# Kernel tuning notes

Hardware: AMD Instinct MI355X
Metric: run time of the kernel (lower is better)

Reference implementation:

```python
import math
import jax, jax.numpy as jnp
import numpy as np

V, S, D, H, L, DS = 256, 1024, 768, 12, 4, 3
B = 4
PEN, EW, FW, RW = 1.0, 0.01, 0.01, 0.01


def setup_inputs():
    ks = jax.random.split(jax.random.key(0), 12)
    std = 0.02
    return {
        "idx": jax.random.randint(ks[0], (B, S), 0, V),
        "targets": jax.random.randint(ks[1], (B, S), 0, V),
        "token_emb": jax.random.normal(ks[2], (V, D)) * std,
        "pos_emb": jax.random.normal(ks[3], (S, D)) * std,
        "token_positions": jax.random.normal(ks[4], (V, DS)) * 0.3,
        "pos_proj_w": jax.random.normal(ks[5], (DS, D)) * std,
        "ln1_g": jnp.ones((L, D)), "ln1_b": jnp.zeros((L, D)),
        "Wqkv": jax.random.normal(ks[6], (L, D, 3 * D)) * std,
        "Wproj": jax.random.normal(ks[7], (L, D, D)) * std,
        "ln2_g": jnp.ones((L, D)), "ln2_b": jnp.zeros((L, D)),
        "Wff1": jax.random.normal(ks[8], (L, D, 4 * D)) * std,
        "bff1": jnp.zeros((L, 4 * D)),
        "Wff2": jax.random.normal(ks[9], (L, 4 * D, D)) * std,
        "bff2": jnp.zeros((L, D)),
        "lnf_g": jnp.ones((D,)), "lnf_b": jnp.zeros((D,)),
    }


def _ln(x, g, b, eps=1e-5):
    m = x.mean(-1, keepdims=True)
    v = ((x - m) ** 2).mean(-1, keepdims=True)
    return (x - m) * jax.lax.rsqrt(v + eps) * g + b


def _forward(idx, targets, p):
    Bv, T = idx.shape
    dh = D // H
    x = p["token_emb"][idx] + p["pos_emb"][jnp.arange(T)]
    seq_pos = p["token_positions"][idx]  # (B,T,3)
    diff = seq_pos[:, :, None, :] - seq_pos[:, None, :, :]
    token_dists = jnp.sqrt((diff ** 2).sum(-1) + 1e-12)  # (B,T,T)
    x = x + seq_pos @ p["pos_proj_w"]
    mask = jnp.triu(jnp.ones((T, T), dtype=bool), k=1)

    def block(carry, lp):
        x, de, fe = carry
        ln1g, ln1b, Wqkv, Wproj, ln2g, ln2b, W1, b1, W2, b2 = lp
        h = _ln(x, ln1g, ln1b)
        q, k, v = jnp.split(h @ Wqkv, 3, axis=-1)
        q = q.reshape(Bv, T, H, dh).transpose(0, 2, 1, 3)
        k = k.reshape(Bv, T, H, dh).transpose(0, 2, 1, 3)
        v = v.reshape(Bv, T, H, dh).transpose(0, 2, 1, 3)
        logits = jnp.einsum('bhid,bhjd->bhij', q, k) / math.sqrt(dh)
        logits = logits - PEN * token_dists[:, None]
        logits = jnp.where(mask, -jnp.inf, logits)
        w = jax.nn.softmax(logits, axis=-1)  # (B,H,T,T)
        de = de + (w * token_dists[:, None]).sum(-1).mean()
        fe = fe + (-(w * jnp.log(w + 1e-9)).sum(-1)).mean()
        o = jnp.einsum('bhij,bhjd->bhid', w, v).transpose(0, 2, 1, 3).reshape(Bv, T, D)
        x = x + o @ Wproj
        h2 = _ln(x, ln2g, ln2b)
        x = x + jax.nn.gelu(h2 @ W1 + b1, approximate=False) @ W2 + b2
        return (x, de, fe), None

    lps = (p["ln1_g"], p["ln1_b"], p["Wqkv"], p["Wproj"], p["ln2_g"], p["ln2_b"],
           p["Wff1"], p["bff1"], p["Wff2"], p["bff2"])
    zero = jnp.zeros((), x.dtype)
    (x, de, fe), _ = jax.lax.scan(block, (x, zero, zero), lps)
    x = _ln(x, p["lnf_g"], p["lnf_b"])
    logits = x @ p["token_emb"].T  # tied lm_head
    pv = p["token_positions"]
    dmat = jnp.sqrt(((pv[:, None] - pv[None]) ** 2).sum(-1) + 1e-12)
    off = ~jnp.eye(V, dtype=bool)
    rep = jnp.where(off, 1.0 / (dmat + 1e-4), 0.0).sum() / (V * (V - 1))
    logp = jax.nn.log_softmax(logits, -1)
    ce = -jnp.take_along_axis(logp, targets[..., None], -1).mean()
    loss = ce + EW * de + FW * fe + RW * rep
    return logits, loss, de, fe, rep


PNAMES = ("token_emb", "pos_emb", "token_positions", "pos_proj_w", "ln1_g", "ln1_b",
          "Wqkv", "Wproj", "ln2_g", "ln2_b", "Wff1", "bff1", "Wff2", "bff2", "lnf_g", "lnf_b")


def reference(idx, targets, token_emb, pos_emb, token_positions, pos_proj_w,
              ln1_g, ln1_b, Wqkv, Wproj, ln2_g, ln2_b,
              Wff1, bff1, Wff2, bff2, lnf_g, lnf_b):
    p = dict(zip(PNAMES, (token_emb, pos_emb, token_positions, pos_proj_w, ln1_g, ln1_b,
                          Wqkv, Wproj, ln2_g, ln2_b, Wff1, bff1, Wff2, bff2, lnf_g, lnf_b)))
    return _forward(idx, targets, p)
```

## Files before the change

kernel.cpp:

```cpp
#include <hip/hip_runtime.h>
#include <math.h>

#define V_   256
#define S_   1024
#define D_   768
#define H_   12
#define L_   4
#define DS_  3
#define B_   4
#define DH_  64
#define BS_  (B_*S_)
#define D3_  (3*D_)
#define D4_  (4*D_)
#define BSV_ (BS_*V_)

typedef __attribute__((ext_vector_type(8))) short short8;
typedef __attribute__((ext_vector_type(4))) float f32x4;

__device__ __forceinline__ ushort f2bf(float f) {
    unsigned u = __float_as_uint(f);
    u = (u + 0x7fffu + ((u >> 16) & 1u)) >> 16;
    return (ushort)u;
}

__device__ __forceinline__ float block_sum(float v, float* red) {
    #pragma unroll
    for (int m = 32; m > 0; m >>= 1) v += __shfl_xor(v, m, 64);
    int wid = threadIdx.x >> 6;
    __syncthreads();
    if ((threadIdx.x & 63) == 0) red[wid] = v;
    __syncthreads();
    return red[0] + red[1] + red[2] + red[3];
}

__device__ __forceinline__ float block_max(float v, float* red) {
    #pragma unroll
    for (int m = 32; m > 0; m >>= 1) v = fmaxf(v, __shfl_xor(v, m, 64));
    int wid = threadIdx.x >> 6;
    __syncthreads();
    if ((threadIdx.x & 63) == 0) red[wid] = v;
    __syncthreads();
    return fmaxf(fmaxf(red[0], red[1]), fmaxf(red[2], red[3]));
}

__global__ void zero_kernel(float* acc) {
    if (threadIdx.x < 8) acc[threadIdx.x] = 0.0f;
}

__global__ __launch_bounds__(256) void embed_kernel(
    const int* __restrict__ idx, const float* __restrict__ tok_emb,
    const float* __restrict__ pos_emb, const float* __restrict__ tok_pos,
    const float* __restrict__ pproj, float* __restrict__ x, float* __restrict__ sp)
{
    int r = blockIdx.x;
    int t = r & (S_ - 1);
    int id = idx[r];
    float s0 = tok_pos[id*3+0], s1 = tok_pos[id*3+1], s2 = tok_pos[id*3+2];
    if (threadIdx.x == 0) { sp[r*3+0] = s0; sp[r*3+1] = s1; sp[r*3+2] = s2; }
    for (int d = threadIdx.x; d < D_; d += 256) {
        x[(size_t)r*D_ + d] = tok_emb[(size_t)id*D_ + d] + pos_emb[(size_t)t*D_ + d]
                            + s0*pproj[d] + s1*pproj[D_+d] + s2*pproj[2*D_+d];
    }
}

template<int OUT>
__global__ __launch_bounds__(256) void ln_kernel(
    const float* __restrict__ in, const float* __restrict__ g,
    const float* __restrict__ b, void* __restrict__ outv)
{
    __shared__ float red[4];
    int r = blockIdx.x, tid = threadIdx.x;
    const float* p = in + (size_t)r*D_;
    float v0 = p[tid], v1 = p[tid+256], v2 = p[tid+512];
    float s = block_sum(v0+v1+v2, red);
    float mean = s * (1.0f/768.0f);
    float d0 = v0-mean, d1 = v1-mean, d2 = v2-mean;
    float var = block_sum(d0*d0+d1*d1+d2*d2, red) * (1.0f/768.0f);
    float inv = rsqrtf(var + 1e-5f);
    float o0 = d0*inv*g[tid    ] + b[tid    ];
    float o1 = d1*inv*g[tid+256] + b[tid+256];
    float o2 = d2*inv*g[tid+512] + b[tid+512];
    if (OUT == 0) {
        float* o = (float*)outv + (size_t)r*D_;
        o[tid] = o0; o[tid+256] = o1; o[tid+512] = o2;
    } else {
        ushort* o = (ushort*)outv + (size_t)r*D_;
        o[tid] = f2bf(o0); o[tid+256] = f2bf(o1); o[tid+512] = f2bf(o2);
    }
}

__global__ __launch_bounds__(256) void transpose_bf16_kernel(
    const float* __restrict__ W, ushort* __restrict__ Wt, int K, int N)
{
    __shared__ float t[32][33];
    int n0 = blockIdx.x * 32, k0 = blockIdx.y * 32;
    int tx = threadIdx.x & 31, ty = threadIdx.x >> 5;
    #pragma unroll
    for (int r = 0; r < 32; r += 8)
        t[ty+r][tx] = W[(size_t)(k0+ty+r)*N + n0 + tx];
    __syncthreads();
    #pragma unroll
    for (int r = 0; r < 32; r += 8)
        Wt[(size_t)(n0+ty+r)*K + k0 + tx] = f2bf(t[tx][ty+r]);
}

template<int EPI>
__global__ __launch_bounds__(256) void gemm_bf16_kernel(
    const ushort* __restrict__ A, const ushort* __restrict__ Bt,
    const float* __restrict__ bias, const float* __restrict__ res,
    void* __restrict__ Cout, void* __restrict__ aux, int M, int N, int K)
{
    __shared__ ushort As[128*32];
    __shared__ ushort Bs[128*32];
    int tid = threadIdx.x;
    int w = tid >> 6, l = tid & 63;
    int bm = blockIdx.y * 128, bn = blockIdx.x * 128;
    int wm = (w >> 1) * 64, wn = (w & 1) * 64;

    f32x4 acc[4][4];
    #pragma unroll
    for (int i = 0; i < 4; ++i)
        #pragma unroll
        for (int j = 0; j < 4; ++j) { acc[i][j][0]=0.f; acc[i][j][1]=0.f; acc[i][j][2]=0.f; acc[i][j][3]=0.f; }

    int rl = l >> 2;
    int sg = (l & 3) ^ ((rl >> 1) & 3);
    const ushort* ap0 = A  + (size_t)(bm + (w*2  )*16 + rl)*K + sg*8;
    const ushort* ap1 = A  + (size_t)(bm + (w*2+1)*16 + rl)*K + sg*8;
    const ushort* bp0 = Bt + (size_t)(bn + (w*2  )*16 + rl)*K + sg*8;
    const ushort* bp1 = Bt + (size_t)(bn + (w*2+1)*16 + rl)*K + sg*8;
    ushort* al0 = &As[(w*2  )*512];
    ushort* al1 = &As[(w*2+1)*512];
    ushort* bl0 = &Bs[(w*2  )*512];
    ushort* bl1 = &Bs[(w*2+1)*512];

    #define STAGE(K0) do { \
        __builtin_amdgcn_global_load_lds((const __attribute__((address_space(1))) void*)(ap0 + (K0)), (__attribute__((address_space(3))) void*)al0, 16, 0, 0); \
        __builtin_amdgcn_global_load_lds((const __attribute__((address_space(1))) void*)(ap1 + (K0)), (__attribute__((address_space(3))) void*)al1, 16, 0, 0); \
        __builtin_amdgcn_global_load_lds((const __attribute__((address_space(1))) void*)(bp0 + (K0)), (__attribute__((address_space(3))) void*)bl0, 16, 0, 0); \
        __builtin_amdgcn_global_load_lds((const __attribute__((address_space(1))) void*)(bp1 + (K0)), (__attribute__((address_space(3))) void*)bl1, 16, 0, 0); \
    } while (0)

    int lq = l & 15, lg = l >> 4;
    STAGE(0);

    for (int k0 = 0; k0 < K; k0 += 32) {
        __syncthreads();
        short8 af[4], bfv[4];
        #pragma unroll
        for (int mi = 0; mi < 4; ++mi) {
            int r = wm + mi*16 + lq;
            int ks = lg ^ ((r >> 1) & 3);
            af[mi] = *(const short8*)&As[r*32 + ks*8];
        }
        #pragma unroll
        for (int ni = 0; ni < 4; ++ni) {
            int r = wn + ni*16 + lq;
            int ks = lg ^ ((r >> 1) & 3);
            bfv[ni] = *(const short8*)&Bs[r*32 + ks*8];
        }
        #pragma unroll
        for (int mi = 0; mi < 4; ++mi)
            #pragma unroll
            for (int ni = 0; ni < 4; ++ni)
                acc[mi][ni] = __builtin_amdgcn_mfma_f32_16x16x32_bf16(af[mi], bfv[ni], acc[mi][ni], 0, 0, 0);
        __syncthreads();
        if (k0 + 32 < K) STAGE(k0 + 32);
    }
    #undef STAGE

    int lr = (l >> 4) * 4;
    #pragma unroll
    for (int mi = 0; mi < 4; ++mi) {
        #pragma unroll
        for (int ni = 0; ni < 4; ++ni) {
            int col = bn + wn + ni*16 + lq;
            int row = bm + wm + mi*16 + lr;
            if (EPI == 4) {
                if (col < 1536) {
                    #pragma unroll
                    for (int q = 0; q < 4; ++q)
                        ((ushort*)Cout)[(size_t)(row+q)*1536 + col] = f2bf(acc[mi][ni][q]);
                } else {
                    int bb = row >> 10, t0 = row & 1023;
                    ushort4 pv = make_ushort4(f2bf(acc[mi][ni][0]), f2bf(acc[mi][ni][1]),
                                              f2bf(acc[mi][ni][2]), f2bf(acc[mi][ni][3]));
                    *(ushort4*)&((ushort*)aux)[((size_t)(bb*768) + (col-1536))*1024 + t0] = pv;
                }
            } else {
                #pragma unroll
                for (int q = 0; q < 4; ++q) {
                    size_t o = (size_t)(row + q)*N + col;
                    float v = acc[mi][ni][q];
                    if (EPI == 0) {
                        ((float*)Cout)[o] = v;
                    } else if (EPI == 1) {
                        ((float*)Cout)[o] = v + res[o];
                    } else if (EPI == 2) {
                        float t = v + bias[col];
                        ((ushort*)Cout)[o] = f2bf(0.5f*t*(1.0f + erff(t*0.70710678118f)));
                    } else {
                        ((float*)Cout)[o] = v + bias[col] + res[o];
                    }
                }
            }
        }
    }
}

template<int EPI, bool BT>
__global__ __launch_bounds__(256) void gemm_kernel(
    const float* __restrict__ A, const float* __restrict__ Bm,
    const float* __restrict__ bias, const float* __restrict__ res,
    float* __restrict__ C, int M, int N, int K)
{
    __shared__ float As[16][68];
    __shared__ float Bs[16][68];
    int tid = threadIdx.x;
    int tx = tid & 15, ty = tid >> 4;
    int bn = blockIdx.x * 64, bm = blockIdx.y * 64;
    float acc[4][4] = {};

    int arow = tid >> 2;
    int akc  = (tid & 3) * 4;
    int kb   = tid >> 4;
    int nb   = (tid & 15) * 4;

    for (int k0 = 0; k0 < K; k0 += 16) {
        float4 av = *(const float4*)&A[(size_t)(bm+arow)*K + k0 + akc];
        As[akc+0][arow] = av.x; As[akc+1][arow] = av.y;
        As[akc+2][arow] = av.z; As[akc+3][arow] = av.w;
        if (!BT) {
            float4 bv = *(const float4*)&Bm[(size_t)(k0+kb)*N + bn + nb];
            *(float4*)&Bs[kb][nb] = bv;
        } else {
            float4 bv = *(const float4*)&Bm[(size_t)(bn+arow)*K + k0 + akc];
            Bs[akc+0][arow] = bv.x; Bs[akc+1][arow] = bv.y;
            Bs[akc+2][arow] = bv.z; Bs[akc+3][arow] = bv.w;
        }
        __syncthreads();
        #pragma unroll
        for (int kk = 0; kk < 16; ++kk) {
            float4 a = *(const float4*)&As[kk][ty*4];
            float4 b = *(const float4*)&Bs[kk][tx*4];
            acc[0][0] += a.x*b.x; acc[0][1] += a.x*b.y; acc[0][2] += a.x*b.z; acc[0][3] += a.x*b.w;
            acc[1][0] += a.y*b.x; acc[1][1] += a.y*b.y; acc[1][2] += a.y*b.z; acc[1][3] += a.y*b.w;
            acc[2][0] += a.z*b.x; acc[2][1] += a.z*b.y; acc[2][2] += a.z*b.z; acc[2][3] += a.z*b.w;
            acc[3][0] += a.w*b.x; acc[3][1] += a.w*b.y; acc[3][2] += a.w*b.z; acc[3][3] += a.w*b.w;
        }
        __syncthreads();
    }

    int row0 = bm + ty*4, col0 = bn + tx*4;
    #pragma unroll
    for (int mm = 0; mm < 4; ++mm) {
        int r = row0 + mm;
        float4 vv = make_float4(acc[mm][0], acc[mm][1], acc[mm][2], acc[mm][3]);
        if (EPI == 1) {
            float4 rr = *(const float4*)&res[(size_t)r*N + col0];
            vv.x += rr.x; vv.y += rr.y; vv.z += rr.z; vv.w += rr.w;
        }
        *(float4*)&C[(size_t)r*N + col0] = vv;
    }
}

__device__ __forceinline__ int swz64(int r, int c) {
    return (r << 6) + ((((c >> 3) ^ (r & 7))) << 3) + (c & 7);
}

__device__ __forceinline__ void stage64(const ushort* __restrict__ g, int gstride,
                                        ushort* lds, int tid) {
    #pragma unroll
    for (int it = 0; it < 2; ++it) {
        int s = tid + it*256;
        int r = s >> 3, cs = (s & 7) << 3;
        short8 v = *(const short8*)&g[(size_t)r*gstride + cs];
        *(short8*)&lds[swz64(r, cs)] = v;
    }
}

__global__ __launch_bounds__(256) void attn_mfma_kernel(
    const ushort* __restrict__ qkb, const ushort* __restrict__ vtb,
    const float* __restrict__ sp,
    ushort* __restrict__ obuf, float* __restrict__ de_acc, float* __restrict__ fe_acc)
{
    __shared__ ushort Qs[64*64];
    __shared__ ushort Ks[64*64];
    __shared__ ushort Vts[64*64];
    __shared__ ushort Ps[64*64];
    __shared__ float sps[64][4];

    int tile = blockIdx.x & 15;
    int h = (blockIdx.x >> 4) % H_;
    int b = blockIdx.x / (16 * H_);
    int i0 = tile * 64;

    int tid = threadIdx.x, w = tid >> 6, l = tid & 63;
    int lq = l & 15, lg = l >> 4;
    int w16 = w * 16;

    stage64(qkb + (size_t)(b*S_ + i0)*1536 + h*64, 1536, Qs, tid);

    float sq0[4], sq1[4], sq2[4];
    #pragma unroll
    for (int q = 0; q < 4; ++q) {
        int i = i0 + w16 + lg*4 + q;
        sq0[q] = sp[(b*S_+i)*3+0];
        sq1[q] = sp[(b*S_+i)*3+1];
        sq2[q] = sp[(b*S_+i)*3+2];
    }

    float M[4], Z[4], Sde[4], Sws[4];
    f32x4 O[4];
    #pragma unroll
    for (int q = 0; q < 4; ++q) { M[q] = -1e30f; Z[q] = 0.f; Sde[q] = 0.f; Sws[q] = 0.f; }
    #pragma unroll
    for (int n = 0; n < 4; ++n) { O[n][0]=0.f; O[n][1]=0.f; O[n][2]=0.f; O[n][3]=0.f; }

    const ushort* kbase = qkb + 768 + h*64;
    const ushort* vbase = vtb + (size_t)((b*H_ + h)*DH_)*S_;

    for (int j0 = 0; j0 <= i0; j0 += 64) {
        __syncthreads();
        stage64(kbase + (size_t)(b*S_ + j0)*1536, 1536, Ks, tid);
        stage64(vbase + j0, S_, Vts, tid);
        if (tid < 64) {
            sps[tid][0] = sp[(b*S_+j0+tid)*3+0];
            sps[tid][1] = sp[(b*S_+j0+tid)*3+1];
            sps[tid][2] = sp[(b*S_+j0+tid)*3+2];
        }
        __syncthreads();

        f32x4 sacc[4];
        #pragma unroll
        for (int n = 0; n < 4; ++n) { sacc[n][0]=0.f; sacc[n][1]=0.f; sacc[n][2]=0.f; sacc[n][3]=0.f; }
        short8 aq0 = *(const short8*)&Qs[swz64(w16+lq, lg*8)];
        short8 aq1 = *(const short8*)&Qs[swz64(w16+lq, 32+lg*8)];
        #pragma unroll
        for (int n = 0; n < 4; ++n) {
            short8 bk0 = *(const short8*)&Ks[swz64(n*16+lq, lg*8)];
            short8 bk1 = *(const short8*)&Ks[swz64(n*16+lq, 32+lg*8)];
            sacc[n] = __builtin_amdgcn_mfma_f32_16x16x32_bf16(aq0, bk0, sacc[n], 0, 0, 0);
            sacc[n] = __builtin_amdgcn_mfma_f32_16x16x32_bf16(aq1, bk1, sacc[n], 0, 0, 0);
        }

        float dstv[4][4], ev[4][4];
        #pragma unroll
        for (int n = 0; n < 4; ++n) {
            float c0 = sps[n*16+lq][0], c1 = sps[n*16+lq][1], c2 = sps[n*16+lq][2];
            int j = j0 + n*16 + lq;
            #pragma unroll
            for (int q = 0; q < 4; ++q) {
                float e0 = sq0[q]-c0, e1 = sq1[q]-c1, e2 = sq2[q]-c2;
                float dist = sqrtf(e0*e0 + e1*e1 + e2*e2 + 1e-12f);
                dstv[n][q] = dist;
                float s = sacc[n][q]*0.125f - dist;
                sacc[n][q] = (j <= i0 + w16 + lg*4 + q) ? s : -1e30f;
            }
        }
        #pragma unroll
        for (int q = 0; q < 4; ++q) {
            float mt = fmaxf(fmaxf(sacc[0][q], sacc[1][q]), fmaxf(sacc[2][q], sacc[3][q]));
            mt = fmaxf(mt, __shfl_xor(mt, 1, 64));
            mt = fmaxf(mt, __shfl_xor(mt, 2, 64));
            mt = fmaxf(mt, __shfl_xor(mt, 4, 64));
            mt = fmaxf(mt, __shfl_xor(mt, 8, 64));
            float Mn = fmaxf(M[q], mt);
            float scale = __expf(M[q] - Mn);
            float zl = 0.f, del = 0.f, wsl = 0.f;
            #pragma unroll
            for (int n = 0; n < 4; ++n) {
                float e = __expf(sacc[n][q] - Mn);
                ev[n][q] = e;
                zl += e; del += e*dstv[n][q]; wsl += e*sacc[n][q];
            }
            zl  += __shfl_xor(zl, 1, 64);  zl  += __shfl_xor(zl, 2, 64);
            zl  += __shfl_xor(zl, 4, 64);  zl  += __shfl_xor(zl, 8, 64);
            del += __shfl_xor(del, 1, 64); del += __shfl_xor(del, 2, 64);
            del += __shfl_xor(del, 4, 64); del += __shfl_xor(del, 8, 64);
            wsl += __shfl_xor(wsl, 1, 64); wsl += __shfl_xor(wsl, 2, 64);
            wsl += __shfl_xor(wsl, 4, 64); wsl += __shfl_xor(wsl, 8, 64);
            Z[q]   = Z[q]  *scale + zl;
            Sde[q] = Sde[q]*scale + del;
            Sws[q] = Sws[q]*scale + wsl;
            M[q] = Mn;
            O[0][q] *= scale; O[1][q] *= scale; O[2][q] *= scale; O[3][q] *= scale;
        }

        #pragma unroll
        for (int n = 0; n < 4; ++n)
            #pragma unroll
            for (int q = 0; q < 4; ++q)
                Ps[swz64(w16 + lg*4 + q, n*16 + lq)] = f2bf(ev[n][q]);
        __syncthreads();

        short8 pa0 = *(const short8*)&Ps[swz64(w16+lq, lg*8)];
        short8 pa1 = *(const short8*)&Ps[swz64(w16+lq, 32+lg*8)];
        #pragma unroll
        for (int n = 0; n < 4; ++n) {
            short8 v0 = *(const short8*)&Vts[swz64(n*16+lq, lg*8)];
            short8 v1 = *(const short8*)&Vts[swz64(n*16+lq, 32+lg*8)];
            O[n] = __builtin_amdgcn_mfma_f32_16x16x32_bf16(pa0, v0, O[n], 0, 0, 0);
            O[n] = __builtin_amdgcn_mfma_f32_16x16x32_bf16(pa1, v1, O[n], 0, 0, 0);
        }
    }

    #pragma unroll
    for (int q = 0; q < 4; ++q) {
        float invz = 1.0f / Z[q];
        int i = i0 + w16 + lg*4 + q;
        ushort* op = obuf + (size_t)(b*S_ + i)*D_ + h*DH_ + lq;
        op[0]  = f2bf(O[0][q]*invz);
        op[16] = f2bf(O[1][q]*invz);
        op[32] = f2bf(O[2][q]*invz);
        op[48] = f2bf(O[3][q]*invz);
    }

    float dsum = 0.f, fsum = 0.f;
    if (lq == 0) {
        #pragma unroll
        for (int q = 0; q < 4; ++q) {
            dsum += Sde[q] / Z[q];
            fsum += M[q] + __logf(Z[q]) - Sws[q] / Z[q];
        }
    }
    #pragma unroll
    for (int m = 32; m > 0; m >>= 1) {
        dsum += __shfl_xor(dsum, m, 64);
        fsum += __shfl_xor(fsum, m, 64);
    }
    if (l == 0) {
        atomicAdd(de_acc, dsum * (1.0f/49152.0f));
        atomicAdd(fe_acc, fsum * (1.0f/49152.0f));
    }
}

__global__ __launch_bounds__(256) void ce_kernel(
    const float* __restrict__ logits, const int* __restrict__ targets,
    float* __restrict__ ce_acc)
{
    __shared__ float red[4];
    int r = blockIdx.x, tid = threadIdx.x;
    float x = logits[(size_t)r*V_ + tid];
    float m = block_max(x, red);
    float e = __expf(x - m);
    float s = block_sum(e, red);
    if (tid == 0) {
        float lse = m + __logf(s);
        float tl = logits[(size_t)r*V_ + targets[r]];
        atomicAdd(ce_acc, (lse - tl) * (1.0f/(float)BS_));
    }
}

__global__ __launch_bounds__(256) void rep_kernel(
    const float* __restrict__ tp, float* __restrict__ rep_acc)
{
    __shared__ float red[4];
    int i = blockIdx.x, j = threadIdx.x;
    float val = 0.0f;
    if (i != j) {
        float d0 = tp[i*3+0]-tp[j*3+0];
        float d1 = tp[i*3+1]-tp[j*3+1];
        float d2 = tp[i*3+2]-tp[j*3+2];
        float dm = sqrtf(d0*d0 + d1*d1 + d2*d2 + 1e-12f);
        val = 1.0f/(dm + 1e-4f);
    }
    float s = block_sum(val, red);
    if (j == 0) atomicAdd(rep_acc, s);
}

__global__ void finalize_kernel(float* __restrict__ out4, const float* __restrict__ acc) {
    if (threadIdx.x == 0) {
        float de = acc[0], fe = acc[1];
        float rep = acc[2] * (1.0f/(256.0f*255.0f));
        float ce = acc[3];
        out4[0] = ce + 0.01f*de + 0.01f*fe + 0.01f*rep;
        out4[1] = de;
        out4[2] = fe;
        out4[3] = rep;
    }
}

extern "C" void kernel_launch(void* const* d_in, const int* in_sizes, int n_in,
                              void* d_out, int out_size, void* d_ws, size_t ws_size,
                              hipStream_t stream)
{
    const int*   idx      = (const int*)  d_in[0];
    const int*   targets  = (const int*)  d_in[1];
    const float* tok_emb  = (const float*)d_in[2];
    const float* pos_emb  = (const float*)d_in[3];
    const float* tok_pos  = (const float*)d_in[4];
    const float* pproj    = (const float*)d_in[5];
    const float* ln1_g    = (const float*)d_in[6];
    const float* ln1_b    = (const float*)d_in[7];
    const float* Wqkv     = (const float*)d_in[8];
    const float* Wproj    = (const float*)d_in[9];
    const float* ln2_g    = (const float*)d_in[10];
    const float* ln2_b    = (const float*)d_in[11];
    const float* Wff1     = (const float*)d_in[12];
    const float* bff1     = (const float*)d_in[13];
    const float* Wff2     = (const float*)d_in[14];
    const float* bff2     = (const float*)d_in[15];
    const float* lnf_g    = (const float*)d_in[16];
    const float* lnf_b    = (const float*)d_in[17];

    float* out = (float*)d_out;

    float* wsf  = (float*)d_ws;
    float* acc  = wsf;
    float* sp   = wsf + 8;
    float* x    = sp + 12288;
    float* hf   = x + (size_t)BS_*D_;
    ushort* hbf  = (ushort*)(hf + (size_t)BS_*D_);
    ushort* ffbf = hbf + (size_t)BS_*D_;
    ushort* qkb  = ffbf + (size_t)BS_*D4_;
    ushort* vtb  = qkb + (size_t)BS_*1536;
    ushort* wqT  = vtb + (size_t)3072*1024;
    ushort* wpT  = wqT + (size_t)D3_*D_;
    ushort* w1T  = wpT + (size_t)D_*D_;
    ushort* w2T  = w1T + (size_t)D4_*D_;

    zero_kernel<<<1, 64, 0, stream>>>(acc);
    embed_kernel<<<BS_, 256, 0, stream>>>(idx, tok_emb, pos_emb, tok_pos, pproj, x, sp);

    for (int l = 0; l < L_; ++l) {
        transpose_bf16_kernel<<<dim3(D3_/32, D_/32), 256, 0, stream>>>(Wqkv + (size_t)l*D_*D3_, wqT, D_, D3_);
        transpose_bf16_kernel<<<dim3(D_/32,  D_/32), 256, 0, stream>>>(Wproj + (size_t)l*D_*D_, wpT, D_, D_);
        transpose_bf16_kernel<<<dim3(D4_/32, D_/32), 256, 0, stream>>>(Wff1 + (size_t)l*D_*D4_, w1T, D_, D4_);
        transpose_bf16_kernel<<<dim3(D_/32, D4_/32), 256, 0, stream>>>(Wff2 + (size_t)l*D4_*D_, w2T, D4_, D_);

        ln_kernel<1><<<BS_, 256, 0, stream>>>(x, ln1_g + l*D_, ln1_b + l*D_, hbf);

        gemm_bf16_kernel<4><<<dim3(D3_/128, BS_/128), 256, 0, stream>>>(
            hbf, wqT, nullptr, nullptr, qkb, vtb, BS_, D3_, D_);

        attn_mfma_kernel<<<B_*H_*(S_/64), 256, 0, stream>>>(qkb, vtb, sp, hbf, &acc[0], &acc[1]);

        gemm_bf16_kernel<1><<<dim3(D_/128, BS_/128), 256, 0, stream>>>(
            hbf, wpT, nullptr, x, x, nullptr, BS_, D_, D_);

        ln_kernel<1><<<BS_, 256, 0, stream>>>(x, ln2_g + l*D_, ln2_b + l*D_, hbf);

        gemm_bf16_kernel<2><<<dim3(D4_/128, BS_/128), 256, 0, stream>>>(
            hbf, w1T, bff1 + (size_t)l*D4_, nullptr, ffbf, nullptr, BS_, D4_, D_);

        gemm_bf16_kernel<3><<<dim3(D_/128, BS_/128), 256, 0, stream>>>(
            ffbf, w2T, bff2 + (size_t)l*D_, x, x, nullptr, BS_, D_, D4_);
    }

    ln_kernel<0><<<BS_, 256, 0, stream>>>(x, lnf_g, lnf_b, hf);

    gemm_kernel<0,true><<<dim3(V_/64, BS_/64), 256, 0, stream>>>(
        hf, tok_emb, nullptr, nullptr, out, BS_, V_, D_);

    ce_kernel<<<BS_, 256, 0, stream>>>(out, targets, &acc[3]);
    rep_kernel<<<V_, 256, 0, stream>>>(tok_pos, &acc[2]);
    finalize_kernel<<<1, 64, 0, stream>>>(out + BSV_, acc);
}
```

Baseline: 1.507 ms.

## Double-buffer attention K/V tiles and merge per-layer weight transposes

The attention kernel now prefetches the next K/V/position tile into registers while computing on the current one. It writes them into a second LDS buffer after the PV MFMA, which removes one block barrier per iteration and the barrier between the P write and read. The causal mask is applied only on the diagonal tile. The cross-lane softmax-sum shuffles are deferred to the end, since the partial sums share the same row max. The four per-layer weight transpose launches are merged into one kernel, and the extra LDS buffers and prefetch registers may reduce occupancy.

```diff
diff --git a/kernel.cpp b/kernel.cpp
--- a/kernel.cpp
+++ b/kernel.cpp
@@ -89,11 +89,21 @@
     }
 }
 
-__global__ __launch_bounds__(256) void transpose_bf16_kernel(
-    const float* __restrict__ W, ushort* __restrict__ Wt, int K, int N)
-{
+__global__ __launch_bounds__(256) void transpose_all_kernel(
+    const float* __restrict__ Wq, const float* __restrict__ Wp,
+    const float* __restrict__ W1, const float* __restrict__ W2,
+    ushort* __restrict__ wqT, ushort* __restrict__ wpT,
+    ushort* __restrict__ w1T, ushort* __restrict__ w2T)
+{
+    int bid = blockIdx.x;
+    const float* W; ushort* Wt; int K, N, nx;
+    if (bid < 1728)      { W = Wq; Wt = wqT; K = 768;  N = 2304; nx = 72; }
+    else if (bid < 2304) { bid -= 1728; W = Wp; Wt = wpT; K = 768;  N = 768;  nx = 24; }
+    else if (bid < 4608) { bid -= 2304; W = W1; Wt = w1T; K = 768;  N = 3072; nx = 96; }
+    else                 { bid -= 4608; W = W2; Wt = w2T; K = 3072; N = 768;  nx = 24; }
+
     __shared__ float t[32][33];
-    int n0 = blockIdx.x * 32, k0 = blockIdx.y * 32;
+    int n0 = (bid % nx) * 32, k0 = (bid / nx) * 32;
     int tx = threadIdx.x & 31, ty = threadIdx.x >> 5;
     #pragma unroll
     for (int r = 0; r < 32; r += 8)
@@ -268,15 +278,17 @@
     return (r << 6) + ((((c >> 3) ^ (r & 7))) << 3) + (c & 7);
 }
 
-__device__ __forceinline__ void stage64(const ushort* __restrict__ g, int gstride,
-                                        ushort* lds, int tid) {
-    #pragma unroll
-    for (int it = 0; it < 2; ++it) {
-        int s = tid + it*256;
-        int r = s >> 3, cs = (s & 7) << 3;
-        short8 v = *(const short8*)&g[(size_t)r*gstride + cs];
-        *(short8*)&lds[swz64(r, cs)] = v;
-    }
+__device__ __forceinline__ void stg_load(const ushort* __restrict__ g, int gstride,
+                                         int tid, short8& va, short8& vb) {
+    int s1 = tid + 256;
+    va = *(const short8*)&g[(size_t)(tid >> 3)*gstride + ((tid & 7) << 3)];
+    vb = *(const short8*)&g[(size_t)(s1  >> 3)*gstride + ((s1  & 7) << 3)];
+}
+
+__device__ __forceinline__ void stg_write(ushort* lds, int tid, short8 va, short8 vb) {
+    int s1 = tid + 256;
+    *(short8*)&lds[swz64(tid >> 3, (tid & 7) << 3)] = va;
+    *(short8*)&lds[swz64(s1  >> 3, (s1  & 7) << 3)] = vb;
 }
 
 __global__ __launch_bounds__(256) void attn_mfma_kernel(
@@ -285,10 +297,10 @@
     ushort* __restrict__ obuf, float* __restrict__ de_acc, float* __restrict__ fe_acc)
 {
     __shared__ ushort Qs[64*64];
-    __shared__ ushort Ks[64*64];
-    __shared__ ushort Vts[64*64];
+    __shared__ ushort Ks[2][64*64];
+    __shared__ ushort Vts[2][64*64];
     __shared__ ushort Ps[64*64];
-    __shared__ float sps[64][4];
+    __shared__ float sps[2][64][4];
 
     int tile = blockIdx.x & 15;
     int h = (blockIdx.x >> 4) % H_;
@@ -299,7 +311,24 @@
     int lq = l & 15, lg = l >> 4;
     int w16 = w * 16;
 
-    stage64(qkb + (size_t)(b*S_ + i0)*1536 + h*64, 1536, Qs, tid);
+    const ushort* kbase = qkb + 768 + h*64;
+    const ushort* vbase = vtb + (size_t)((b*H_ + h)*DH_)*S_;
+
+    {
+        short8 qa, qb2;
+        stg_load(qkb + (size_t)(b*S_ + i0)*1536 + h*64, 1536, tid, qa, qb2);
+        stg_write(Qs, tid, qa, qb2);
+        short8 ka, kb2, va, vb2;
+        stg_load(kbase + (size_t)(b*S_)*1536, 1536, tid, ka, kb2);
+        stg_load(vbase, S_, tid, va, vb2);
+        stg_write(Ks[0], tid, ka, kb2);
+        stg_write(Vts[0], tid, va, vb2);
+        if (tid < 64) {
+            sps[0][tid][0] = sp[(b*S_+tid)*3+0];
+            sps[0][tid][1] = sp[(b*S_+tid)*3+1];
+            sps[0][tid][2] = sp[(b*S_+tid)*3+2];
+        }
+    }
 
     float sq0[4], sq1[4], sq2[4];
     #pragma unroll
@@ -310,26 +339,29 @@
         sq2[q] = sp[(b*S_+i)*3+2];
     }
 
-    float M[4], Z[4], Sde[4], Sws[4];
+    float M[4], Zp[4], Sdep[4], Swsp[4];
     f32x4 O[4];
     #pragma unroll
-    for (int q = 0; q < 4; ++q) { M[q] = -1e30f; Z[q] = 0.f; Sde[q] = 0.f; Sws[q] = 0.f; }
+    for (int q = 0; q < 4; ++q) { M[q] = -1e30f; Zp[q] = 0.f; Sdep[q] = 0.f; Swsp[q] = 0.f; }
     #pragma unroll
     for (int n = 0; n < 4; ++n) { O[n][0]=0.f; O[n][1]=0.f; O[n][2]=0.f; O[n][3]=0.f; }
 
-    const ushort* kbase = qkb + 768 + h*64;
-    const ushort* vbase = vtb + (size_t)((b*H_ + h)*DH_)*S_;
-
-    for (int j0 = 0; j0 <= i0; j0 += 64) {
+    int cur = 0;
+    for (int j0 = 0; j0 <= i0; j0 += 64, cur ^= 1) {
         __syncthreads();
-        stage64(kbase + (size_t)(b*S_ + j0)*1536, 1536, Ks, tid);
-        stage64(vbase + j0, S_, Vts, tid);
-        if (tid < 64) {
-            sps[tid][0] = sp[(b*S_+j0+tid)*3+0];
-            sps[tid][1] = sp[(b*S_+j0+tid)*3+1];
-            sps[tid][2] = sp[(b*S_+j0+tid)*3+2];
-        }
-        __syncthreads();
+
+        bool haveNext = (j0 + 64 <= i0);
+        short8 nka, nkb, nva, nvb;
+        float ns0 = 0.f, ns1 = 0.f, ns2 = 0.f;
+        if (haveNext) {
+            stg_load(kbase + (size_t)(b*S_ + j0 + 64)*1536, 1536, tid, nka, nkb);
+            stg_load(vbase + j0 + 64, S_, tid, nva, nvb);
+            if (tid < 64) {
+                ns0 = sp[(b*S_+j0+64+tid)*3+0];
+                ns1 = sp[(b*S_+j0+64+tid)*3+1];
+                ns2 = sp[(b*S_+j0+64+tid)*3+2];
+            }
+        }
 
         f32x4 sacc[4];
         #pragma unroll
@@ -338,26 +370,35 @@
         short8 aq1 = *(const short8*)&Qs[swz64(w16+lq, 32+lg*8)];
         #pragma unroll
         for (int n = 0; n < 4; ++n) {
-            short8 bk0 = *(const short8*)&Ks[swz64(n*16+lq, lg*8)];
-            short8 bk1 = *(const short8*)&Ks[swz64(n*16+lq, 32+lg*8)];
+            short8 bk0 = *(const short8*)&Ks[cur][swz64(n*16+lq, lg*8)];
+            short8 bk1 = *(const short8*)&Ks[cur][swz64(n*16+lq, 32+lg*8)];
             sacc[n] = __builtin_amdgcn_mfma_f32_16x16x32_bf16(aq0, bk0, sacc[n], 0, 0, 0);
             sacc[n] = __builtin_amdgcn_mfma_f32_16x16x32_bf16(aq1, bk1, sacc[n], 0, 0, 0);
         }
 
-        float dstv[4][4], ev[4][4];
+        float dstv[4][4];
         #pragma unroll
         for (int n = 0; n < 4; ++n) {
-            float c0 = sps[n*16+lq][0], c1 = sps[n*16+lq][1], c2 = sps[n*16+lq][2];
-            int j = j0 + n*16 + lq;
+            float c0 = sps[cur][n*16+lq][0], c1 = sps[cur][n*16+lq][1], c2 = sps[cur][n*16+lq][2];
             #pragma unroll
             for (int q = 0; q < 4; ++q) {
                 float e0 = sq0[q]-c0, e1 = sq1[q]-c1, e2 = sq2[q]-c2;
                 float dist = sqrtf(e0*e0 + e1*e1 + e2*e2 + 1e-12f);
                 dstv[n][q] = dist;
-                float s = sacc[n][q]*0.125f - dist;
-                sacc[n][q] = (j <= i0 + w16 + lg*4 + q) ? s : -1e30f;
+                sacc[n][q] = sacc[n][q]*0.125f - dist;
             }
         }
+        if (j0 == i0) {
+            #pragma unroll
+            for (int n = 0; n < 4; ++n) {
+                int j = j0 + n*16 + lq;
+                #pragma unroll
+                for (int q = 0; q < 4; ++q)
+                    sacc[n][q] = (j <= i0 + w16 + lg*4 + q) ? sacc[n][q] : -1e30f;
+            }
+        }
+
+        float ev[4][4];
         #pragma unroll
         for (int q = 0; q < 4; ++q) {
             float mt = fmaxf(fmaxf(sacc[0][q], sacc[1][q]), fmaxf(sacc[2][q], sacc[3][q]));
@@ -367,22 +408,16 @@
             mt = fmaxf(mt, __shfl_xor(mt, 8, 64));
             float Mn = fmaxf(M[q], mt);
             float scale = __expf(M[q] - Mn);
-            float zl = 0.f, del = 0.f, wsl = 0.f;
+            float zl = 0.f, dl = 0.f, wl = 0.f;
             #pragma unroll
             for (int n = 0; n < 4; ++n) {
                 float e = __expf(sacc[n][q] - Mn);
                 ev[n][q] = e;
-                zl += e; del += e*dstv[n][q]; wsl += e*sacc[n][q];
+                zl += e; dl += e*dstv[n][q]; wl += e*sacc[n][q];
             }
-            zl  += __shfl_xor(zl, 1, 64);  zl  += __shfl_xor(zl, 2, 64);
-            zl  += __shfl_xor(zl, 4, 64);  zl  += __shfl_xor(zl, 8, 64);
-            del += __shfl_xor(del, 1, 64); del += __shfl_xor(del, 2, 64);
-            del += __shfl_xor(del, 4, 64); del += __shfl_xor(del, 8, 64);
-            wsl += __shfl_xor(wsl, 1, 64); wsl += __shfl_xor(wsl, 2, 64);
-            wsl += __shfl_xor(wsl, 4, 64); wsl += __shfl_xor(wsl, 8, 64);
-            Z[q]   = Z[q]  *scale + zl;
-            Sde[q] = Sde[q]*scale + del;
-            Sws[q] = Sws[q]*scale + wsl;
+            Zp[q]   = Zp[q]  *scale + zl;
+            Sdep[q] = Sdep[q]*scale + dl;
+            Swsp[q] = Swsp[q]*scale + wl;
             M[q] = Mn;
             O[0][q] *= scale; O[1][q] *= scale; O[2][q] *= scale; O[3][q] *= scale;
         }
@@ -392,17 +427,39 @@
             #pragma unroll
             for (int q = 0; q < 4; ++q)
                 Ps[swz64(w16 + lg*4 + q, n*16 + lq)] = f2bf(ev[n][q]);
-        __syncthreads();
 
         short8 pa0 = *(const short8*)&Ps[swz64(w16+lq, lg*8)];
         short8 pa1 = *(const short8*)&Ps[swz64(w16+lq, 32+lg*8)];
         #pragma unroll
         for (int n = 0; n < 4; ++n) {
-            short8 v0 = *(const short8*)&Vts[swz64(n*16+lq, lg*8)];
-            short8 v1 = *(const short8*)&Vts[swz64(n*16+lq, 32+lg*8)];
+            short8 v0 = *(const short8*)&Vts[cur][swz64(n*16+lq, lg*8)];
+            short8 v1 = *(const short8*)&Vts[cur][swz64(n*16+lq, 32+lg*8)];
             O[n] = __builtin_amdgcn_mfma_f32_16x16x32_bf16(pa0, v0, O[n], 0, 0, 0);
             O[n] = __builtin_amdgcn_mfma_f32_16x16x32_bf16(pa1, v1, O[n], 0, 0, 0);
         }
+
+        if (haveNext) {
+            stg_write(Ks[cur^1], tid, nka, nkb);
+            stg_write(Vts[cur^1], tid, nva, nvb);
+            if (tid < 64) {
+                sps[cur^1][tid][0] = ns0;
+                sps[cur^1][tid][1] = ns1;
+                sps[cur^1][tid][2] = ns2;
+            }
+        }
+    }
+
+    float Z[4], Sde[4], Sws[4];
+    #pragma unroll
+    for (int q = 0; q < 4; ++q) {
+        float z = Zp[q], d = Sdep[q], ws = Swsp[q];
+        z += __shfl_xor(z, 1, 64); z += __shfl_xor(z, 2, 64);
+        z += __shfl_xor(z, 4, 64); z += __shfl_xor(z, 8, 64);
+        d += __shfl_xor(d, 1, 64); d += __shfl_xor(d, 2, 64);
+        d += __shfl_xor(d, 4, 64); d += __shfl_xor(d, 8, 64);
+        ws += __shfl_xor(ws, 1, 64); ws += __shfl_xor(ws, 2, 64);
+        ws += __shfl_xor(ws, 4, 64); ws += __shfl_xor(ws, 8, 64);
+        Z[q] = z; Sde[q] = d; Sws[q] = ws;
     }
 
     #pragma unroll
@@ -524,10 +581,10 @@
     embed_kernel<<<BS_, 256, 0, stream>>>(idx, tok_emb, pos_emb, tok_pos, pproj, x, sp);
 
     for (int l = 0; l < L_; ++l) {
-        transpose_bf16_kernel<<<dim3(D3_/32, D_/32), 256, 0, stream>>>(Wqkv + (size_t)l*D_*D3_, wqT, D_, D3_);
-        transpose_bf16_kernel<<<dim3(D_/32,  D_/32), 256, 0, stream>>>(Wproj + (size_t)l*D_*D_, wpT, D_, D_);
-        transpose_bf16_kernel<<<dim3(D4_/32, D_/32), 256, 0, stream>>>(Wff1 + (size_t)l*D_*D4_, w1T, D_, D4_);
-        transpose_bf16_kernel<<<dim3(D_/32, D4_/32), 256, 0, stream>>>(Wff2 + (size_t)l*D4_*D_, w2T, D4_, D_);
+        transpose_all_kernel<<<6912, 256, 0, stream>>>(
+            Wqkv + (size_t)l*D_*D3_, Wproj + (size_t)l*D_*D_,
+            Wff1 + (size_t)l*D_*D4_, Wff2 + (size_t)l*D4_*D_,
+            wqT, wpT, w1T, w2T);
 
         ln_kernel<1><<<BS_, 256, 0, stream>>>(x, ln1_g + l*D_, ln1_b + l*D_, hbf);
 
```

New measurement: 1.536 ms. Within noise of the previous version (+1.9%).

## Split causal attention over key chunks with a combine pass; merge weight transposes

Applied to the files above, without the earlier changes.

Attention now splits each query tile's causal key range into up to four 256-key chunks, each handled by its own block. Each block writes partial max/sum statistics and an unnormalised bf16 output, and a new combine kernel merges the chunks and reduces the de/fe losses. This is meant to fix the load imbalance of causal tiles and raise parallelism. The cost is an extra launch and extra global traffic, and the partial outputs are rounded to bf16 before merging. The chunk kernel also applies the causal mask only on the diagonal tile, moves the row-sum shuffles out of the key loop, and drops a barrier before reading P. The four per-layer weight transpose launches are merged into one kernel.

```diff
diff --git a/kernel.cpp b/kernel.cpp
--- a/kernel.cpp
+++ b/kernel.cpp
@@ -21,6 +21,9 @@
     unsigned u = __float_as_uint(f);
     u = (u + 0x7fffu + ((u >> 16) & 1u)) >> 16;
     return (ushort)u;
+}
+__device__ __forceinline__ float bf2f(ushort u) {
+    return __uint_as_float(((unsigned)u) << 16);
 }
 
 __device__ __forceinline__ float block_sum(float v, float* red) {
@@ -89,11 +92,21 @@
     }
 }
 
-__global__ __launch_bounds__(256) void transpose_bf16_kernel(
-    const float* __restrict__ W, ushort* __restrict__ Wt, int K, int N)
-{
+__global__ __launch_bounds__(256) void transpose_all_kernel(
+    const float* __restrict__ Wq, const float* __restrict__ Wp,
+    const float* __restrict__ W1, const float* __restrict__ W2,
+    ushort* __restrict__ wqT, ushort* __restrict__ wpT,
+    ushort* __restrict__ w1T, ushort* __restrict__ w2T)
+{
+    int bid = blockIdx.x;
+    const float* W; ushort* Wt; int K, N, nx;
+    if (bid < 1728)      { W = Wq; Wt = wqT; K = 768;  N = 2304; nx = 72; }
+    else if (bid < 2304) { bid -= 1728; W = Wp; Wt = wpT; K = 768;  N = 768;  nx = 24; }
+    else if (bid < 4608) { bid -= 2304; W = W1; Wt = w1T; K = 768;  N = 3072; nx = 96; }
+    else                 { bid -= 4608; W = W2; Wt = w2T; K = 3072; N = 768;  nx = 24; }
+
     __shared__ float t[32][33];
-    int n0 = blockIdx.x * 32, k0 = blockIdx.y * 32;
+    int n0 = (bid % nx) * 32, k0 = (bid / nx) * 32;
     int tx = threadIdx.x & 31, ty = threadIdx.x >> 5;
     #pragma unroll
     for (int r = 0; r < 32; r += 8)
@@ -279,25 +292,31 @@
     }
 }
 
-__global__ __launch_bounds__(256) void attn_mfma_kernel(
+__global__ __launch_bounds__(256) void attn_chunk_kernel(
     const ushort* __restrict__ qkb, const ushort* __restrict__ vtb,
     const float* __restrict__ sp,
-    ushort* __restrict__ obuf, float* __restrict__ de_acc, float* __restrict__ fe_acc)
-{
+    float4* __restrict__ pstats, ushort* __restrict__ popart)
+{
+    int t  = blockIdx.x;
+    int hb = blockIdx.y;
+    int ci = blockIdx.z;
+    if (ci > (t >> 2)) return;
+    int b = hb / H_, h = hb % H_;
+    int i0 = t * 64;
+    int slot = (hb * 16 + t) * 4 + ci;
+
     __shared__ ushort Qs[64*64];
     __shared__ ushort Ks[64*64];
     __shared__ ushort Vts[64*64];
     __shared__ ushort Ps[64*64];
     __shared__ float sps[64][4];
 
-    int tile = blockIdx.x & 15;
-    int h = (blockIdx.x >> 4) % H_;
-    int b = blockIdx.x / (16 * H_);
-    int i0 = tile * 64;
-
     int tid = threadIdx.x, w = tid >> 6, l = tid & 63;
     int lq = l & 15, lg = l >> 4;
     int w16 = w * 16;
+
+    const ushort* kbase = qkb + 768 + h*64;
+    const ushort* vbase = vtb + (size_t)((b*H_ + h)*DH_)*S_;
 
     stage64(qkb + (size_t)(b*S_ + i0)*1536 + h*64, 1536, Qs, tid);
 
@@ -310,17 +329,18 @@
         sq2[q] = sp[(b*S_+i)*3+2];
     }
 
-    float M[4], Z[4], Sde[4], Sws[4];
+    float M[4], Zp[4], Sdep[4], Swsp[4];
     f32x4 O[4];
     #pragma unroll
-    for (int q = 0; q < 4; ++q) { M[q] = -1e30f; Z[q] = 0.f; Sde[q] = 0.f; Sws[q] = 0.f; }
+    for (int q = 0; q < 4; ++q) { M[q] = -1e30f; Zp[q] = 0.f; Sdep[q] = 0.f; Swsp[q] = 0.f; }
     #pragma unroll
     for (int n = 0; n < 4; ++n) { O[n][0]=0.f; O[n][1]=0.f; O[n][2]=0.f; O[n][3]=0.f; }
 
-    const ushort* kbase = qkb + 768 + h*64;
-    const ushort* vbase = vtb + (size_t)((b*H_ + h)*DH_)*S_;
-
-    for (int j0 = 0; j0 <= i0; j0 += 64) {
+    int jbeg = ci * 256;
+    int jend0 = jbeg + 256;
+    int jend = (jend0 < i0 + 64) ? jend0 : (i0 + 64);
+
+    for (int j0 = jbeg; j0 < jend; j0 += 64) {
         __syncthreads();
         stage64(kbase + (size_t)(b*S_ + j0)*1536, 1536, Ks, tid);
         stage64(vbase + j0, S_, Vts, tid);
@@ -344,20 +364,29 @@
             sacc[n] = __builtin_amdgcn_mfma_f32_16x16x32_bf16(aq1, bk1, sacc[n], 0, 0, 0);
         }
 
-        float dstv[4][4], ev[4][4];
+        float dstv[4][4];
         #pragma unroll
         for (int n = 0; n < 4; ++n) {
             float c0 = sps[n*16+lq][0], c1 = sps[n*16+lq][1], c2 = sps[n*16+lq][2];
-            int j = j0 + n*16 + lq;
             #pragma unroll
             for (int q = 0; q < 4; ++q) {
                 float e0 = sq0[q]-c0, e1 = sq1[q]-c1, e2 = sq2[q]-c2;
                 float dist = sqrtf(e0*e0 + e1*e1 + e2*e2 + 1e-12f);
                 dstv[n][q] = dist;
-                float s = sacc[n][q]*0.125f - dist;
-                sacc[n][q] = (j <= i0 + w16 + lg*4 + q) ? s : -1e30f;
+                sacc[n][q] = sacc[n][q]*0.125f - dist;
             }
         }
+        if (j0 == i0) {
+            #pragma unroll
+            for (int n = 0; n < 4; ++n) {
+                int j = j0 + n*16 + lq;
+                #pragma unroll
+                for (int q = 0; q < 4; ++q)
+                    sacc[n][q] = (j <= i0 + w16 + lg*4 + q) ? sacc[n][q] : -1e30f;
+            }
+        }
+
+        float ev[4][4];
         #pragma unroll
         for (int q = 0; q < 4; ++q) {
             float mt = fmaxf(fmaxf(sacc[0][q], sacc[1][q]), fmaxf(sacc[2][q], sacc[3][q]));
@@ -367,22 +396,16 @@
             mt = fmaxf(mt, __shfl_xor(mt, 8, 64));
             float Mn = fmaxf(M[q], mt);
             float scale = __expf(M[q] - Mn);
-            float zl = 0.f, del = 0.f, wsl = 0.f;
+            float zl = 0.f, dl = 0.f, wl = 0.f;
             #pragma unroll
             for (int n = 0; n < 4; ++n) {
                 float e = __expf(sacc[n][q] - Mn);
                 ev[n][q] = e;
-                zl += e; del += e*dstv[n][q]; wsl += e*sacc[n][q];
+                zl += e; dl += e*dstv[n][q]; wl += e*sacc[n][q];
             }
-            zl  += __shfl_xor(zl, 1, 64);  zl  += __shfl_xor(zl, 2, 64);
-            zl  += __shfl_xor(zl, 4, 64);  zl  += __shfl_xor(zl, 8, 64);
-            del += __shfl_xor(del, 1, 64); del += __shfl_xor(del, 2, 64);
-            del += __shfl_xor(del, 4, 64); del += __shfl_xor(del, 8, 64);
-            wsl += __shfl_xor(wsl, 1, 64); wsl += __shfl_xor(wsl, 2, 64);
-            wsl += __shfl_xor(wsl, 4, 64); wsl += __shfl_xor(wsl, 8, 64);
-            Z[q]   = Z[q]  *scale + zl;
-            Sde[q] = Sde[q]*scale + del;
-            Sws[q] = Sws[q]*scale + wsl;
+            Zp[q]   = Zp[q]  *scale + zl;
+            Sdep[q] = Sdep[q]*scale + dl;
+            Swsp[q] = Swsp[q]*scale + wl;
             M[q] = Mn;
             O[0][q] *= scale; O[1][q] *= scale; O[2][q] *= scale; O[3][q] *= scale;
         }
@@ -392,7 +415,6 @@
             #pragma unroll
             for (int q = 0; q < 4; ++q)
                 Ps[swz64(w16 + lg*4 + q, n*16 + lq)] = f2bf(ev[n][q]);
-        __syncthreads();
 
         short8 pa0 = *(const short8*)&Ps[swz64(w16+lq, lg*8)];
         short8 pa1 = *(const short8*)&Ps[swz64(w16+lq, 32+lg*8)];
@@ -405,33 +427,84 @@
         }
     }
 
+    float Z[4], Sde[4], Sws[4];
     #pragma unroll
     for (int q = 0; q < 4; ++q) {
-        float invz = 1.0f / Z[q];
-        int i = i0 + w16 + lg*4 + q;
-        ushort* op = obuf + (size_t)(b*S_ + i)*D_ + h*DH_ + lq;
-        op[0]  = f2bf(O[0][q]*invz);
-        op[16] = f2bf(O[1][q]*invz);
-        op[32] = f2bf(O[2][q]*invz);
-        op[48] = f2bf(O[3][q]*invz);
-    }
-
-    float dsum = 0.f, fsum = 0.f;
+        float z = Zp[q], d = Sdep[q], ws = Swsp[q];
+        z += __shfl_xor(z, 1, 64); z += __shfl_xor(z, 2, 64);
+        z += __shfl_xor(z, 4, 64); z += __shfl_xor(z, 8, 64);
+        d += __shfl_xor(d, 1, 64); d += __shfl_xor(d, 2, 64);
+        d += __shfl_xor(d, 4, 64); d += __shfl_xor(d, 8, 64);
+        ws += __shfl_xor(ws, 1, 64); ws += __shfl_xor(ws, 2, 64);
+        ws += __shfl_xor(ws, 4, 64); ws += __shfl_xor(ws, 8, 64);
+        Z[q] = z; Sde[q] = d; Sws[q] = ws;
+    }
+
     if (lq == 0) {
         #pragma unroll
-        for (int q = 0; q < 4; ++q) {
-            dsum += Sde[q] / Z[q];
-            fsum += M[q] + __logf(Z[q]) - Sws[q] / Z[q];
-        }
-    }
-    #pragma unroll
-    for (int m = 32; m > 0; m >>= 1) {
-        dsum += __shfl_xor(dsum, m, 64);
-        fsum += __shfl_xor(fsum, m, 64);
-    }
-    if (l == 0) {
-        atomicAdd(de_acc, dsum * (1.0f/49152.0f));
-        atomicAdd(fe_acc, fsum * (1.0f/49152.0f));
+        for (int q = 0; q < 4; ++q)
+            pstats[(size_t)slot*64 + w16 + lg*4 + q] = make_float4(M[q], Z[q], Sde[q], Sws[q]);
+    }
+    #pragma unroll
+    for (int q = 0; q < 4; ++q) {
+        int row = w16 + lg*4 + q;
+        #pragma unroll
+        for (int n = 0; n < 4; ++n)
+            popart[(size_t)slot*4096 + row*64 + n*16 + lq] = f2bf(O[n][q]);
+    }
+}
+
+__global__ __launch_bounds__(256) void attn_combine_kernel(
+    const float4* __restrict__ pstats, const ushort* __restrict__ popart,
+    ushort* __restrict__ obuf, float* __restrict__ de_acc, float* __restrict__ fe_acc)
+{
+    __shared__ float red[4];
+    int t = blockIdx.x, hb = blockIdx.y;
+    int b = hb / H_, h = hb % H_;
+    int nch = (t >> 2) + 1;
+    int tid = threadIdx.x;
+    int r = tid >> 2;
+    int dg = (tid & 3) << 4;
+    int slot0 = (hb*16 + t) * 4;
+
+    float Mg = -1e30f;
+    for (int c = 0; c < nch; ++c)
+        Mg = fmaxf(Mg, pstats[(size_t)(slot0+c)*64 + r].x);
+
+    float Zt = 0.f, Sdt = 0.f, Swt = 0.f;
+    float Ov[16];
+    #pragma unroll
+    for (int d = 0; d < 16; ++d) Ov[d] = 0.f;
+
+    for (int c = 0; c < nch; ++c) {
+        float4 st = pstats[(size_t)(slot0+c)*64 + r];
+        float wc = __expf(st.x - Mg);
+        Zt += st.y * wc; Sdt += st.z * wc; Swt += st.w * wc;
+        const ushort* po = popart + (size_t)(slot0+c)*4096 + r*64 + dg;
+        short8 p0 = *(const short8*)&po[0];
+        short8 p1 = *(const short8*)&po[8];
+        #pragma unroll
+        for (int d = 0; d < 8; ++d) {
+            Ov[d]   += bf2f((ushort)p0[d]) * wc;
+            Ov[8+d] += bf2f((ushort)p1[d]) * wc;
+        }
+    }
+
+    float invz = 1.0f / Zt;
+    ushort o16[16];
+    #pragma unroll
+    for (int d = 0; d < 16; ++d) o16[d] = f2bf(Ov[d] * invz);
+    ushort* op = obuf + (size_t)(b*S_ + t*64 + r)*D_ + h*DH_ + dg;
+    *(uint4*)&op[0] = *(uint4*)&o16[0];
+    *(uint4*)&op[8] = *(uint4*)&o16[8];
+
+    float de = ((tid & 3) == 0) ? Sdt * invz : 0.f;
+    float fe = ((tid & 3) == 0) ? (Mg + __logf(Zt) - Swt * invz) : 0.f;
+    float des = block_sum(de, red);
+    float fes = block_sum(fe, red);
+    if (tid == 0) {
+        atomicAdd(de_acc, des * (1.0f/49152.0f));
+        atomicAdd(fe_acc, fes * (1.0f/49152.0f));
     }
 }
 
@@ -511,7 +584,8 @@
     float* sp   = wsf + 8;
     float* x    = sp + 12288;
     float* hf   = x + (size_t)BS_*D_;
-    ushort* hbf  = (ushort*)(hf + (size_t)BS_*D_);
+    float* pstats_f = hf + (size_t)BS_*D_;
+    ushort* hbf  = (ushort*)(pstats_f + (size_t)3072*64*4);
     ushort* ffbf = hbf + (size_t)BS_*D_;
     ushort* qkb  = ffbf + (size_t)BS_*D4_;
     ushort* vtb  = qkb + (size_t)BS_*1536;
@@ -519,22 +593,27 @@
     ushort* wpT  = wqT + (size_t)D3_*D_;
     ushort* w1T  = wpT + (size_t)D_*D_;
     ushort* w2T  = w1T + (size_t)D4_*D_;
+    float4* pstats = (float4*)pstats_f;
+    ushort* popart = ffbf;
 
     zero_kernel<<<1, 64, 0, stream>>>(acc);
     embed_kernel<<<BS_, 256, 0, stream>>>(idx, tok_emb, pos_emb, tok_pos, pproj, x, sp);
 
     for (int l = 0; l < L_; ++l) {
-        transpose_bf16_kernel<<<dim3(D3_/32, D_/32), 256, 0, stream>>>(Wqkv + (size_t)l*D_*D3_, wqT, D_, D3_);
-        transpose_bf16_kernel<<<dim3(D_/32,  D_/32), 256, 0, stream>>>(Wproj + (size_t)l*D_*D_, wpT, D_, D_);
-        transpose_bf16_kernel<<<dim3(D4_/32, D_/32), 256, 0, stream>>>(Wff1 + (size_t)l*D_*D4_, w1T, D_, D4_);
-        transpose_bf16_kernel<<<dim3(D_/32, D4_/32), 256, 0, stream>>>(Wff2 + (size_t)l*D4_*D_, w2T, D4_, D_);
+        transpose_all_kernel<<<6912, 256, 0, stream>>>(
+            Wqkv + (size_t)l*D_*D3_, Wproj + (size_t)l*D_*D_,
+            Wff1 + (size_t)l*D_*D4_, Wff2 + (size_t)l*D4_*D_,
+            wqT, wpT, w1T, w2T);
 
         ln_kernel<1><<<BS_, 256, 0, stream>>>(x, ln1_g + l*D_, ln1_b + l*D_, hbf);
 
         gemm_bf16_kernel<4><<<dim3(D3_/128, BS_/128), 256, 0, stream>>>(
             hbf, wqT, nullptr, nullptr, qkb, vtb, BS_, D3_, D_);
 
-        attn_mfma_kernel<<<B_*H_*(S_/64), 256, 0, stream>>>(qkb, vtb, sp, hbf, &acc[0], &acc[1]);
+        attn_chunk_kernel<<<dim3(16, B_*H_, 4), 256, 0, stream>>>(
+            qkb, vtb, sp, pstats, popart);
+        attn_combine_kernel<<<dim3(16, B_*H_), 256, 0, stream>>>(
+            pstats, popart, hbf, &acc[0], &acc[1]);
 
         gemm_bf16_kernel<1><<<dim3(D_/128, BS_/128), 256, 0, stream>>>(
             hbf, wpT, nullptr, x, x, nullptr, BS_, D_, D_);
```

Measured after the change: 1.611 ms. +6.9%, slower.
